# Kernel optimization log

Measured on AMD Instinct MI355X. Metric: run time of the kernel, lower is better.

## Reference

```python
import jax, jax.numpy as jnp
import numpy as np

LA, LB, D = 4096, 4096, 1024

def setup_inputs() -> dict:
    key = jax.random.key(0)
    ka, kb = jax.random.split(key)
    a_hat = jax.random.normal(ka, (LA, D), dtype=jnp.float32)
    b_hat = jax.random.normal(kb, (LB, D), dtype=jnp.float32)
    return {"a_hat": a_hat, "b_hat": b_hat}

def _m_vector(v_hat, v_wave):
    # concat along dim 0, matching torch.concat(..., dim=0)
    return jnp.concatenate((v_hat, v_wave, v_hat - v_wave, v_hat * v_wave), axis=0)

def reference(a_hat, b_hat):
    # energy: [La, Lb]
    energy = jnp.matmul(a_hat, b_hat.T)
    # softmax over columns (dim 1) -> attend over b rows
    wave_a = jnp.matmul(jax.nn.softmax(energy, axis=1), b_hat)      # [La, D]
    # softmax over rows (dim 0), transposed -> attend over a rows
    wave_b = jnp.matmul(jax.nn.softmax(energy, axis=0).T, a_hat)    # [Lb, D]
    m_a = _m_vector(a_hat, wave_a)   # [4*La, D]
    m_b = _m_vector(b_hat, wave_b)   # [4*Lb, D]
    return (m_a, m_b)
```

## Files before the change

kernel.cpp:

```cpp
#include <hip/hip_runtime.h>
#include <cstdint>
#include <cstddef>

#define LA 4096
#define LB 4096
#define DD 1024

typedef unsigned short u16;
typedef short bf16x8 __attribute__((ext_vector_type(8)));
typedef float f32x4 __attribute__((ext_vector_type(4)));

__device__ __forceinline__ u16 f2bf(float f) {
  unsigned u = __builtin_bit_cast(unsigned, f);
  u += 0x7fffu + ((u >> 16) & 1u);
  return (u16)(u >> 16);
}
__device__ __forceinline__ float bf2f(u16 h) {
  return __builtin_bit_cast(float, (unsigned)h << 16);
}
__device__ __forceinline__ void async16(const void* g, void* l) {
  __builtin_amdgcn_global_load_lds(
      (const __attribute__((address_space(1))) unsigned int*)g,
      (__attribute__((address_space(3))) unsigned int*)l, 16, 0, 0);
}

__global__ __launch_bounds__(256) void prep(const float* __restrict__ A,
                                            const float* __restrict__ B,
                                            u16* __restrict__ Ahi, u16* __restrict__ Alo,
                                            u16* __restrict__ Bhi, u16* __restrict__ Blo,
                                            u16* __restrict__ Bt) {
  __shared__ u16 t[32][33];
  const int bx = blockIdx.x;
  const int tid = threadIdx.x;
  if (bx < 4096) {
    const int side = bx >> 11;
    const size_t idx = ((size_t)(bx & 2047) * 256 + tid) * 8;
    const float* src = side ? B : A;
    u16* dh = side ? Bhi : Ahi;
    u16* dl = side ? Blo : Alo;
    const float4 a = *(const float4*)&src[idx];
    const float4 b = *(const float4*)&src[idx + 4];
    float v[8] = {a.x, a.y, a.z, a.w, b.x, b.y, b.z, b.w};
    bf16x8 hi, lo;
#pragma unroll
    for (int i = 0; i < 8; ++i) {
      const u16 h = f2bf(v[i]);
      hi[i] = (short)h;
      lo[i] = (short)f2bf(v[i] - bf2f(h));
    }
    *(bf16x8*)&dh[idx] = hi;
    *(bf16x8*)&dl[idx] = lo;
  } else {
    const int blk = bx - 4096;
    const int c0 = (blk & 31) * 32;
    const int r0 = (blk >> 5) * 32;
    const int lr = tid >> 3, lc = (tid & 7) * 4;
    const float4 v = *(const float4*)&B[(size_t)(r0 + lr) * DD + c0 + lc];
    t[lr][lc + 0] = f2bf(v.x); t[lr][lc + 1] = f2bf(v.y);
    t[lr][lc + 2] = f2bf(v.z); t[lr][lc + 3] = f2bf(v.w);
    __syncthreads();
    ushort4 w;
    w.x = t[lc + 0][lr]; w.y = t[lc + 1][lr]; w.z = t[lc + 2][lr]; w.w = t[lc + 3][lr];
    *(ushort4*)&Bt[(size_t)(c0 + lr) * LB + r0 + lc] = w;
  }
}

__global__ __launch_bounds__(256) void tr_f32(const float* __restrict__ in,
                                              u16* __restrict__ out,
                                              int R, int C) {
  __shared__ u16 t[32][33];
  const int c0 = blockIdx.x * 32, r0 = blockIdx.y * 32;
  const int tid = threadIdx.x;
  const int lr = tid >> 3, lc = (tid & 7) * 4;
  const float4 v = *(const float4*)&in[(size_t)(r0 + lr) * C + c0 + lc];
  t[lr][lc + 0] = f2bf(v.x); t[lr][lc + 1] = f2bf(v.y);
  t[lr][lc + 2] = f2bf(v.z); t[lr][lc + 3] = f2bf(v.w);
  __syncthreads();
  ushort4 w;
  w.x = t[lc + 0][lr]; w.y = t[lc + 1][lr]; w.z = t[lc + 2][lr]; w.w = t[lc + 3][lr];
  *(ushort4*)&out[(size_t)(c0 + lr) * R + r0 + lc] = w;
}

__global__ __launch_bounds__(256) void gemm_energy(const u16* __restrict__ Ahi,
                                                   const u16* __restrict__ Alo,
                                                   const u16* __restrict__ Bhi,
                                                   const u16* __restrict__ Blo,
                                                   float* __restrict__ E,
                                                   float* __restrict__ pmax,
                                                   float* __restrict__ psum) {
  __shared__ u16 lah[128 * 32], lal[128 * 32], lbh[128 * 32], lbl[128 * 32];
  __shared__ float cred[4][4][16][2];
  const int j0 = blockIdx.x * 128;
  const int i0 = blockIdx.y * 128;
  const int tid = threadIdx.x;
  const int lane = tid & 63, quad = lane >> 4, lq = lane & 15;
  const int wave = tid >> 6;
  const int wm = (wave & 1) * 64, wn = (wave >> 1) * 64;
  f32x4 acc[4][4] = {};
  for (int kt = 0; kt < DD; kt += 32) {
    if (kt) __syncthreads();
#pragma unroll
    for (int r = 0; r < 2; ++r) {
      const int chunk = wave * 128 + r * 64 + lane;
      const int row = chunk >> 2;
      const int kc = (chunk & 3) * 8;
      const int lofs = (wave * 128 + r * 64) * 16;
      const size_t ga = (size_t)(i0 + row) * DD + kt + kc;
      const size_t gb = (size_t)(j0 + row) * DD + kt + kc;
      async16(Ahi + ga, (char*)lah + lofs);
      async16(Alo + ga, (char*)lal + lofs);
      async16(Bhi + gb, (char*)lbh + lofs);
      async16(Blo + gb, (char*)lbl + lofs);
    }
    __syncthreads();
    bf16x8 fah[4], fal[4], fbh[4], fbl[4];
#pragma unroll
    for (int f = 0; f < 4; ++f) {
      fah[f] = *(const bf16x8*)&lah[(wm + f * 16 + lq) * 32 + quad * 8];
      fal[f] = *(const bf16x8*)&lal[(wm + f * 16 + lq) * 32 + quad * 8];
      fbh[f] = *(const bf16x8*)&lbh[(wn + f * 16 + lq) * 32 + quad * 8];
      fbl[f] = *(const bf16x8*)&lbl[(wn + f * 16 + lq) * 32 + quad * 8];
    }
#pragma unroll
    for (int fm = 0; fm < 4; ++fm)
#pragma unroll
      for (int fn = 0; fn < 4; ++fn) {
        acc[fm][fn] = __builtin_amdgcn_mfma_f32_16x16x32_bf16(fal[fm], fbh[fn], acc[fm][fn], 0, 0, 0);
        acc[fm][fn] = __builtin_amdgcn_mfma_f32_16x16x32_bf16(fah[fm], fbl[fn], acc[fm][fn], 0, 0, 0);
        acc[fm][fn] = __builtin_amdgcn_mfma_f32_16x16x32_bf16(fah[fm], fbh[fn], acc[fm][fn], 0, 0, 0);
      }
  }
#pragma unroll
  for (int fm = 0; fm < 4; ++fm)
#pragma unroll
    for (int fn = 0; fn < 4; ++fn)
#pragma unroll
      for (int r = 0; r < 4; ++r) {
        const int gi = i0 + wm + fm * 16 + quad * 4 + r;
        const int gj = j0 + wn + fn * 16 + lq;
        E[(size_t)gi * LB + gj] = acc[fm][fn][r];
      }
  const int rg = i0 >> 7;
#pragma unroll
  for (int fn = 0; fn < 4; ++fn) {
    float m = acc[0][fn][0];
#pragma unroll
    for (int fm = 0; fm < 4; ++fm)
#pragma unroll
      for (int r = 0; r < 4; ++r) m = fmaxf(m, acc[fm][fn][r]);
    float s = 0.f;
#pragma unroll
    for (int fm = 0; fm < 4; ++fm)
#pragma unroll
      for (int r = 0; r < 4; ++r) s += __expf(acc[fm][fn][r] - m);
#pragma unroll
    for (int mask = 16; mask <= 32; mask <<= 1) {
      const float om = __shfl_xor(m, mask);
      const float os = __shfl_xor(s, mask);
      const float nm = fmaxf(m, om);
      s = s * __expf(m - nm) + os * __expf(om - nm);
      m = nm;
    }
    if (quad == 0) { cred[wave][fn][lq][0] = m; cred[wave][fn][lq][1] = s; }
  }
  __syncthreads();
  if ((wave & 1) == 0 && quad == 0) {
#pragma unroll
    for (int fn = 0; fn < 4; ++fn) {
      const float m1 = cred[wave][fn][lq][0], s1 = cred[wave][fn][lq][1];
      const float m2 = cred[wave + 1][fn][lq][0], s2 = cred[wave + 1][fn][lq][1];
      const float nm = fmaxf(m1, m2);
      const float s = s1 * __expf(m1 - nm) + s2 * __expf(m2 - nm);
      const int c = j0 + wn + fn * 16 + lq;
      pmax[rg * LB + c] = nm;
      psum[rg * LB + c] = s;
    }
  }
}

__global__ __launch_bounds__(256) void row_softmax_pa(const float* __restrict__ E,
                                                      float* __restrict__ rinv,
                                                      u16* __restrict__ P,
                                                      float* __restrict__ wa) {
  __shared__ float red[8];
  const int row = blockIdx.x, tid = threadIdx.x;
  const float* e = E + (size_t)row * LB;
  float4 v[4];
#pragma unroll
  for (int c = 0; c < 4; ++c) v[c] = *(const float4*)&e[(c * 256 + tid) * 4];
  float m = -__builtin_inff();
#pragma unroll
  for (int c = 0; c < 4; ++c)
    m = fmaxf(m, fmaxf(fmaxf(v[c].x, v[c].y), fmaxf(v[c].z, v[c].w)));
#pragma unroll
  for (int o = 32; o > 0; o >>= 1) m = fmaxf(m, __shfl_down(m, o));
  if ((tid & 63) == 0) red[tid >> 6] = m;
  __syncthreads();
  m = fmaxf(fmaxf(red[0], red[1]), fmaxf(red[2], red[3]));
  float s = 0.f;
#pragma unroll
  for (int c = 0; c < 4; ++c)
    s += __expf(v[c].x - m) + __expf(v[c].y - m) + __expf(v[c].z - m) + __expf(v[c].w - m);
#pragma unroll
  for (int o = 32; o > 0; o >>= 1) s += __shfl_down(s, o);
  if ((tid & 63) == 0) red[4 + (tid >> 6)] = s;
  __syncthreads();
  if (tid == 0) rinv[row] = 1.f / (red[4] + red[5] + red[6] + red[7]);
#pragma unroll
  for (int c = 0; c < 4; ++c) {
    ushort4 w;
    w.x = f2bf(__expf(v[c].x - m));
    w.y = f2bf(__expf(v[c].y - m));
    w.z = f2bf(__expf(v[c].z - m));
    w.w = f2bf(__expf(v[c].w - m));
    *(ushort4*)&P[(size_t)row * LB + (c * 256 + tid) * 4] = w;
  }
  float4 z = {0.f, 0.f, 0.f, 0.f};
  *(float4*)&wa[(size_t)row * DD + tid * 4] = z;
}

__global__ __launch_bounds__(256) void col_combine(const float* __restrict__ pmax,
                                                   const float* __restrict__ psum,
                                                   float* __restrict__ cmax,
                                                   float* __restrict__ cinv) {
  const int c = blockIdx.x * 256 + threadIdx.x;
  float m = -__builtin_inff(), s = 0.f;
#pragma unroll 4
  for (int g = 0; g < 32; ++g) {
    const float pm = pmax[g * LB + c], ps = psum[g * LB + c];
    const float nm = fmaxf(m, pm);
    s = s * __expf(m - nm) + ps * __expf(pm - nm);
    m = nm;
  }
  cmax[c] = m;
  cinv[c] = 1.f / s;
}

__global__ __launch_bounds__(256) void make_pb(const float* __restrict__ E,
                                               const float* __restrict__ cmax,
                                               u16* __restrict__ P) {
  __shared__ u16 t[32][33];
  const int j0 = blockIdx.x * 32;
  const int i0 = blockIdx.y * 32;
  const int tid = threadIdx.x;
  const int lr = tid >> 3, lc = (tid & 7) * 4;
  const float4 v = *(const float4*)&E[(size_t)(i0 + lr) * LB + j0 + lc];
  const float4 cm = *(const float4*)&cmax[j0 + lc];
  t[lr][lc + 0] = f2bf(__expf(v.x - cm.x));
  t[lr][lc + 1] = f2bf(__expf(v.y - cm.y));
  t[lr][lc + 2] = f2bf(__expf(v.z - cm.z));
  t[lr][lc + 3] = f2bf(__expf(v.w - cm.w));
  __syncthreads();
  ushort4 w;
  w.x = t[lc + 0][lr]; w.y = t[lc + 1][lr]; w.z = t[lc + 2][lr]; w.w = t[lc + 3][lr];
  *(ushort4*)&P[(size_t)(j0 + lr) * LA + i0 + lc] = w;
}

template <int ATOMIC>
__global__ __launch_bounds__(256) void gemm_pv(const u16* __restrict__ P,
                                               const u16* __restrict__ Vt,
                                               const float* __restrict__ inv,
                                               float* __restrict__ W0,
                                               float* __restrict__ W1) {
  __shared__ u16 lds_a[128 * 32];
  __shared__ u16 lds_b[128 * 32];
  const int n0 = blockIdx.x * 128;
  const int i0 = blockIdx.y * 128;
  const int kz = blockIdx.z;
  const int tid = threadIdx.x;
  const int lane = tid & 63, quad = lane >> 4, lq = lane & 15;
  const int wave = tid >> 6;
  const int wm = (wave & 1) * 64, wn = (wave >> 1) * 64;
  f32x4 acc[4][4] = {};
  for (int t = 0; t < 64; ++t) {
    const int kt = kz * 2048 + t * 32;
    if (t) __syncthreads();
#pragma unroll
    for (int r = 0; r < 2; ++r) {
      const int chunk = wave * 128 + r * 64 + lane;
      const int row = chunk >> 2;
      const int kc = (chunk & 3) * 8;
      const int lofs = (wave * 128 + r * 64) * 16;
      async16(P + (size_t)(i0 + row) * 4096 + kt + kc, (char*)lds_a + lofs);
      async16(Vt + (size_t)(n0 + row) * 4096 + kt + kc, (char*)lds_b + lofs);
    }
    __syncthreads();
    bf16x8 af[4], bfr[4];
#pragma unroll
    for (int f = 0; f < 4; ++f) {
      af[f]  = *(const bf16x8*)&lds_a[(wm + f * 16 + lq) * 32 + quad * 8];
      bfr[f] = *(const bf16x8*)&lds_b[(wn + f * 16 + lq) * 32 + quad * 8];
    }
#pragma unroll
    for (int fm = 0; fm < 4; ++fm)
#pragma unroll
      for (int fn = 0; fn < 4; ++fn)
        acc[fm][fn] = __builtin_amdgcn_mfma_f32_16x16x32_bf16(af[fm], bfr[fn], acc[fm][fn], 0, 0, 0);
  }
  float* W = ATOMIC ? W0 : (kz ? W1 : W0);
#pragma unroll
  for (int fm = 0; fm < 4; ++fm)
#pragma unroll
    for (int r = 0; r < 4; ++r) {
      const int gm = i0 + wm + fm * 16 + quad * 4 + r;
      const float sc = inv[gm];
#pragma unroll
      for (int fn = 0; fn < 4; ++fn) {
        const int gn = n0 + wn + fn * 16 + lq;
        if (ATOMIC)
          unsafeAtomicAdd(&W[(size_t)gm * DD + gn], acc[fm][fn][r] * sc);
        else
          W[(size_t)gm * DD + gn] = acc[fm][fn][r] * sc;
      }
    }
}

__global__ __launch_bounds__(256) void finish(const float* __restrict__ Ain,
                                              const float* __restrict__ Bin,
                                              const float* __restrict__ p1,
                                              float* __restrict__ out) {
  const int side = blockIdx.x >> 11;
  const int blk = blockIdx.x & 2047;
  const size_t idx = ((size_t)blk * 256 + threadIdx.x) * 8;
  const size_t S = (size_t)LA * DD;
  const float* src = side ? Bin : Ain;
  float* ob = out + (size_t)side * 4 * S;
  const float4 a0 = *(const float4*)&src[idx];
  const float4 a1 = *(const float4*)&src[idx + 4];
  float4 w0 = *(const float4*)&ob[S + idx];
  float4 w1 = *(const float4*)&ob[S + idx + 4];
  if (side) {
    const float4 q0 = *(const float4*)&p1[idx];
    const float4 q1 = *(const float4*)&p1[idx + 4];
    w0.x += q0.x; w0.y += q0.y; w0.z += q0.z; w0.w += q0.w;
    w1.x += q1.x; w1.y += q1.y; w1.z += q1.z; w1.w += q1.w;
    *(float4*)&ob[S + idx] = w0;
    *(float4*)&ob[S + idx + 4] = w1;
  }
  float4 s0, s1, m0, m1;
  s0.x = a0.x - w0.x; s0.y = a0.y - w0.y; s0.z = a0.z - w0.z; s0.w = a0.w - w0.w;
  s1.x = a1.x - w1.x; s1.y = a1.y - w1.y; s1.z = a1.z - w1.z; s1.w = a1.w - w1.w;
  m0.x = a0.x * w0.x; m0.y = a0.y * w0.y; m0.z = a0.z * w0.z; m0.w = a0.w * w0.w;
  m1.x = a1.x * w1.x; m1.y = a1.y * w1.y; m1.z = a1.z * w1.z; m1.w = a1.w * w1.w;
  *(float4*)&ob[idx] = a0;            *(float4*)&ob[idx + 4] = a1;
  *(float4*)&ob[2 * S + idx] = s0;    *(float4*)&ob[2 * S + idx + 4] = s1;
  *(float4*)&ob[3 * S + idx] = m0;    *(float4*)&ob[3 * S + idx + 4] = m1;
}

extern "C" void kernel_launch(void* const* d_in, const int* in_sizes, int n_in,
                              void* d_out, int out_size, void* d_ws, size_t ws_size,
                              hipStream_t stream) {
  const float* A = (const float*)d_in[0];
  const float* B = (const float*)d_in[1];
  float* out = (float*)d_out;
  const size_t S = (size_t)LA * DD;

  float* pmax = out;
  float* psum = pmax + 131072;
  float* rmax = psum + 131072;
  float* rinv = rmax + 4096;
  float* cmax = rinv + 4096;
  float* cinv = cmax + 4096;
  u16*   Bt   = (u16*)(out + 1048576);
  u16*   Ahi  = (u16*)(out + 2 * S);
  u16*   Alo  = Ahi + S;
  u16*   Bhi  = Alo + S;
  u16*   Blo  = Bhi + S;
  u16*   P    = (u16*)(out + 2 * S);
  float* E    = out + 4 * S;
  u16*   At   = (u16*)(out + 4 * S);
  float* wave_a = out + S;
  float* wave_b = out + 5 * S;
  float* pB1    = out + 6 * S;

  prep<<<dim3(8192), 256, 0, stream>>>(A, B, Ahi, Alo, Bhi, Blo, Bt);

  gemm_energy<<<dim3(LB / 128, LA / 128), 256, 0, stream>>>(Ahi, Alo, Bhi, Blo, E, pmax, psum);

  row_softmax_pa<<<dim3(LA), 256, 0, stream>>>(E, rinv, P, wave_a);
  col_combine<<<dim3(LB / 256), 256, 0, stream>>>(pmax, psum, cmax, cinv);

  gemm_pv<1><<<dim3(DD / 128, LA / 128, 2), 256, 0, stream>>>(P, Bt, rinv, wave_a, nullptr);

  make_pb<<<dim3(LB / 32, LA / 32), 256, 0, stream>>>(E, cmax, P);
  tr_f32<<<dim3(DD / 32, LA / 32), 256, 0, stream>>>(A, At, LA, DD);
  gemm_pv<0><<<dim3(DD / 128, LB / 128, 2), 256, 0, stream>>>(P, At, cinv, wave_b, pB1);

  finish<<<dim3(4096), 256, 0, stream>>>(A, B, pB1, out);
}
```

Before: 442.2 us.

## Restructure energy GEMM with concatenated split-bf16 operands and 256x256 pipelined tiles

The split-bf16 hi/lo planes are interleaved into a single K=3072 operand per matrix: A becomes [hi,hi,lo] and B becomes [hi,lo,hi], so the three-product fp32 emulation turns into one plain bf16 GEMM. The energy kernel is rewritten as a 512-thread, 256x256-tile kernel with double-buffered LDS, an XOR swizzle against bank conflicts, interleaved load/MFMA phases with explicit barriers and priority hints, and a block-index swizzle for L2 locality. This targets global/LDS traffic and MFMA under-utilisation in the old 128x128 kernel. The cost is larger prep writes and more complex manual synchronisation, which could hide ordering bugs.

```diff
diff --git a/kernel.cpp b/kernel.cpp
--- a/kernel.cpp
+++ b/kernel.cpp
@@ -26,8 +26,8 @@
 
 __global__ __launch_bounds__(256) void prep(const float* __restrict__ A,
                                             const float* __restrict__ B,
-                                            u16* __restrict__ Ahi, u16* __restrict__ Alo,
-                                            u16* __restrict__ Bhi, u16* __restrict__ Blo,
+                                            u16* __restrict__ Ap,
+                                            u16* __restrict__ Bp,
                                             u16* __restrict__ Bt) {
   __shared__ u16 t[32][33];
   const int bx = blockIdx.x;
@@ -36,8 +36,7 @@
     const int side = bx >> 11;
     const size_t idx = ((size_t)(bx & 2047) * 256 + tid) * 8;
     const float* src = side ? B : A;
-    u16* dh = side ? Bhi : Ahi;
-    u16* dl = side ? Blo : Alo;
+    u16* dst = side ? Bp : Ap;
     const float4 a = *(const float4*)&src[idx];
     const float4 b = *(const float4*)&src[idx + 4];
     float v[8] = {a.x, a.y, a.z, a.w, b.x, b.y, b.z, b.w};
@@ -48,8 +47,12 @@
       hi[i] = (short)h;
       lo[i] = (short)f2bf(v[i] - bf2f(h));
     }
-    *(bf16x8*)&dh[idx] = hi;
-    *(bf16x8*)&dl[idx] = lo;
+    const size_t row = idx >> 10;
+    const size_t k = idx & 1023;
+    u16* base = dst + row * 3072 + k;
+    *(bf16x8*)&base[0] = hi;
+    *(bf16x8*)&base[side ? 2048 : 1024] = hi;
+    *(bf16x8*)&base[side ? 1024 : 2048] = lo;
   } else {
     const int blk = bx - 4096;
     const int c0 = (blk & 31) * 32;
@@ -81,76 +84,140 @@
   *(ushort4*)&out[(size_t)(c0 + lr) * R + r0 + lc] = w;
 }
 
-__global__ __launch_bounds__(256) void gemm_energy(const u16* __restrict__ Ahi,
-                                                   const u16* __restrict__ Alo,
-                                                   const u16* __restrict__ Bhi,
-                                                   const u16* __restrict__ Blo,
-                                                   float* __restrict__ E,
-                                                   float* __restrict__ pmax,
-                                                   float* __restrict__ psum) {
-  __shared__ u16 lah[128 * 32], lal[128 * 32], lbh[128 * 32], lbl[128 * 32];
-  __shared__ float cred[4][4][16][2];
-  const int j0 = blockIdx.x * 128;
-  const int i0 = blockIdx.y * 128;
+#define NTILES 48
+
+#define STAGE(M, h, tt)                                                      \
+  do {                                                                       \
+    if ((tt) < NTILES) {                                                     \
+      u16* lb = &lds[(tt) & 1][M][h][0];                                     \
+      async16(gsrc[M][h][0] + (tt) * 128, lb + ldst0);                       \
+      async16(gsrc[M][h][1] + (tt) * 128, lb + ldst1);                       \
+    }                                                                        \
+  } while (0)
+
+#define LDA(mbase)                                                           \
+  _Pragma("unroll") for (int m = 0; m < 4; ++m)                              \
+  _Pragma("unroll") for (int ks = 0; ks < 2; ++ks) {                         \
+    const int row = (mbase + m) * 16 + lq;                                   \
+    const int cb = (ks * 64 + quad * 16) ^ (((row >> 2) & 1) << 5);          \
+    af[m][ks] = *(const bf16x8*)&lds[p][0][wr][row * 64 + (cb >> 1)];        \
+  }
+
+#define LDB(arr, fbase)                                                      \
+  _Pragma("unroll") for (int f = 0; f < 2; ++f)                              \
+  _Pragma("unroll") for (int ks = 0; ks < 2; ++ks) {                         \
+    const int row = (wc & 1) * 64 + (fbase + f) * 16 + lq;                   \
+    const int cb = (ks * 64 + quad * 16) ^ (((row >> 2) & 1) << 5);          \
+    arr[f][ks] = *(const bf16x8*)&lds[p][1][wc >> 1][row * 64 + (cb >> 1)];  \
+  }
+
+#define MM(mbase, fbase, barr)                                               \
+  __builtin_amdgcn_s_setprio(1);                                             \
+  _Pragma("unroll") for (int m = 0; m < 4; ++m)                              \
+  _Pragma("unroll") for (int f = 0; f < 2; ++f)                              \
+  _Pragma("unroll") for (int ks = 0; ks < 2; ++ks)                           \
+    acc[mbase + m][fbase + f] = __builtin_amdgcn_mfma_f32_16x16x32_bf16(     \
+        af[m][ks], barr[f][ks], acc[mbase + m][fbase + f], 0, 0, 0);         \
+  __builtin_amdgcn_s_setprio(0);
+
+#define SBAR __builtin_amdgcn_s_barrier()
+#define SCHB __builtin_amdgcn_sched_barrier(0)
+#define LGKM0 asm volatile("s_waitcnt lgkmcnt(0)" ::: "memory")
+
+__global__ __launch_bounds__(512, 2) void gemm8ph(const u16* __restrict__ Ap,
+                                                  const u16* __restrict__ Bp,
+                                                  float* __restrict__ E,
+                                                  float* __restrict__ pmax,
+                                                  float* __restrict__ psum) {
+  __shared__ u16 lds[2][2][2][8192];
   const int tid = threadIdx.x;
   const int lane = tid & 63, quad = lane >> 4, lq = lane & 15;
   const int wave = tid >> 6;
-  const int wm = (wave & 1) * 64, wn = (wave >> 1) * 64;
-  f32x4 acc[4][4] = {};
-  for (int kt = 0; kt < DD; kt += 32) {
-    if (kt) __syncthreads();
-#pragma unroll
-    for (int r = 0; r < 2; ++r) {
-      const int chunk = wave * 128 + r * 64 + lane;
-      const int row = chunk >> 2;
-      const int kc = (chunk & 3) * 8;
-      const int lofs = (wave * 128 + r * 64) * 16;
-      const size_t ga = (size_t)(i0 + row) * DD + kt + kc;
-      const size_t gb = (size_t)(j0 + row) * DD + kt + kc;
-      async16(Ahi + ga, (char*)lah + lofs);
-      async16(Alo + ga, (char*)lal + lofs);
-      async16(Bhi + gb, (char*)lbh + lofs);
-      async16(Blo + gb, (char*)lbl + lofs);
-    }
-    __syncthreads();
-    bf16x8 fah[4], fal[4], fbh[4], fbl[4];
-#pragma unroll
-    for (int f = 0; f < 4; ++f) {
-      fah[f] = *(const bf16x8*)&lah[(wm + f * 16 + lq) * 32 + quad * 8];
-      fal[f] = *(const bf16x8*)&lal[(wm + f * 16 + lq) * 32 + quad * 8];
-      fbh[f] = *(const bf16x8*)&lbh[(wn + f * 16 + lq) * 32 + quad * 8];
-      fbl[f] = *(const bf16x8*)&lbl[(wn + f * 16 + lq) * 32 + quad * 8];
-    }
-#pragma unroll
-    for (int fm = 0; fm < 4; ++fm)
-#pragma unroll
-      for (int fn = 0; fn < 4; ++fn) {
-        acc[fm][fn] = __builtin_amdgcn_mfma_f32_16x16x32_bf16(fal[fm], fbh[fn], acc[fm][fn], 0, 0, 0);
-        acc[fm][fn] = __builtin_amdgcn_mfma_f32_16x16x32_bf16(fah[fm], fbl[fn], acc[fm][fn], 0, 0, 0);
-        acc[fm][fn] = __builtin_amdgcn_mfma_f32_16x16x32_bf16(fah[fm], fbh[fn], acc[fm][fn], 0, 0, 0);
+  const int wr = wave >> 2, wc = wave & 3;
+  int lin = blockIdx.y * 16 + blockIdx.x;
+  lin = (lin & 7) * 32 + (lin >> 3);
+  const int j0 = (lin & 15) * 256;
+  const int i0 = (lin >> 4) * 256;
+
+  const char* gsrc[2][2][2];
+  int ldst0, ldst1;
+  {
+    const int db0 = tid * 16, db1 = 8192 + tid * 16;
+    const int dr0 = db0 >> 7, dr1 = db1 >> 7;
+    const int sc0 = (db0 & 127) ^ (((dr0 >> 2) & 1) << 5);
+    const int sc1 = (db1 & 127) ^ (((dr1 >> 2) & 1) << 5);
+    ldst0 = wave * 512;
+    ldst1 = 4096 + wave * 512;
+#pragma unroll
+    for (int M = 0; M < 2; ++M)
+#pragma unroll
+      for (int h = 0; h < 2; ++h) {
+        const char* base = (const char*)(M ? Bp : Ap);
+        const int rb = (M ? j0 : i0) + h * 128;
+        gsrc[M][h][0] = base + (size_t)(rb + dr0) * 6144 + sc0;
+        gsrc[M][h][1] = base + (size_t)(rb + dr1) * 6144 + sc1;
       }
   }
-#pragma unroll
-  for (int fm = 0; fm < 4; ++fm)
+
+  f32x4 acc[8][4] = {};
+  bf16x8 af[4][2], bf0[2][2], bf1[2][2];
+
+  STAGE(1, 0, 0); STAGE(1, 1, 0); STAGE(0, 0, 0); STAGE(0, 1, 0);
+  asm volatile("s_waitcnt vmcnt(4)" ::: "memory");
+  STAGE(1, 0, 1); STAGE(1, 1, 1); STAGE(0, 0, 1);
+  asm volatile("s_waitcnt vmcnt(6)" ::: "memory");
+  SBAR;
+
+  for (int t = 0; t < NTILES; ++t) {
+    const int p = t & 1;
+    SCHB;
+    LDA(0); LDB(bf0, 0);
+    STAGE(0, 1, t + 1);
+    SCHB; SBAR; LGKM0; SCHB;
+    MM(0, 0, bf0);
+    SCHB; SBAR;
+    SCHB;
+    LDB(bf1, 2);
+    STAGE(1, 0, t + 2);
+    SCHB; SBAR; LGKM0; SCHB;
+    MM(0, 2, bf1);
+    SCHB; SBAR;
+    SCHB;
+    LDA(4);
+    STAGE(1, 1, t + 2);
+    SCHB; SBAR; LGKM0; SCHB;
+    MM(4, 0, bf0);
+    SCHB; SBAR;
+    SCHB;
+    STAGE(0, 0, t + 2);
+    SCHB; SBAR; LGKM0; SCHB;
+    MM(4, 2, bf1);
+    SCHB;
+    asm volatile("s_waitcnt vmcnt(6)" ::: "memory");
+    SBAR;
+  }
+
+  const int rbase = i0 + wr * 128;
+  const int cbase = j0 + wc * 64;
+#pragma unroll
+  for (int fm = 0; fm < 8; ++fm)
 #pragma unroll
     for (int fn = 0; fn < 4; ++fn)
 #pragma unroll
-      for (int r = 0; r < 4; ++r) {
-        const int gi = i0 + wm + fm * 16 + quad * 4 + r;
-        const int gj = j0 + wn + fn * 16 + lq;
-        E[(size_t)gi * LB + gj] = acc[fm][fn][r];
-      }
-  const int rg = i0 >> 7;
+      for (int r = 0; r < 4; ++r)
+        E[(size_t)(rbase + fm * 16 + quad * 4 + r) * LB + cbase + fn * 16 + lq] =
+            acc[fm][fn][r];
+  const int rg = (i0 >> 7) + wr;
 #pragma unroll
   for (int fn = 0; fn < 4; ++fn) {
     float m = acc[0][fn][0];
 #pragma unroll
-    for (int fm = 0; fm < 4; ++fm)
+    for (int fm = 0; fm < 8; ++fm)
 #pragma unroll
       for (int r = 0; r < 4; ++r) m = fmaxf(m, acc[fm][fn][r]);
     float s = 0.f;
 #pragma unroll
-    for (int fm = 0; fm < 4; ++fm)
+    for (int fm = 0; fm < 8; ++fm)
 #pragma unroll
       for (int r = 0; r < 4; ++r) s += __expf(acc[fm][fn][r] - m);
 #pragma unroll
@@ -161,19 +228,9 @@
       s = s * __expf(m - nm) + os * __expf(om - nm);
       m = nm;
     }
-    if (quad == 0) { cred[wave][fn][lq][0] = m; cred[wave][fn][lq][1] = s; }
-  }
-  __syncthreads();
-  if ((wave & 1) == 0 && quad == 0) {
-#pragma unroll
-    for (int fn = 0; fn < 4; ++fn) {
-      const float m1 = cred[wave][fn][lq][0], s1 = cred[wave][fn][lq][1];
-      const float m2 = cred[wave + 1][fn][lq][0], s2 = cred[wave + 1][fn][lq][1];
-      const float nm = fmaxf(m1, m2);
-      const float s = s1 * __expf(m1 - nm) + s2 * __expf(m2 - nm);
-      const int c = j0 + wn + fn * 16 + lq;
-      pmax[rg * LB + c] = nm;
-      psum[rg * LB + c] = s;
+    if (quad == 0) {
+      pmax[rg * LB + cbase + fn * 16 + lq] = m;
+      psum[rg * LB + cbase + fn * 16 + lq] = s;
     }
   }
 }
@@ -362,10 +419,8 @@
   float* cmax = rinv + 4096;
   float* cinv = cmax + 4096;
   u16*   Bt   = (u16*)(out + 1048576);
-  u16*   Ahi  = (u16*)(out + 2 * S);
-  u16*   Alo  = Ahi + S;
-  u16*   Bhi  = Alo + S;
-  u16*   Blo  = Bhi + S;
+  u16*   Ap   = (u16*)(out + S);
+  u16*   Bp   = Ap + (size_t)LA * 3072;
   u16*   P    = (u16*)(out + 2 * S);
   float* E    = out + 4 * S;
   u16*   At   = (u16*)(out + 4 * S);
@@ -373,9 +428,9 @@
   float* wave_b = out + 5 * S;
   float* pB1    = out + 6 * S;
 
-  prep<<<dim3(8192), 256, 0, stream>>>(A, B, Ahi, Alo, Bhi, Blo, Bt);
-
-  gemm_energy<<<dim3(LB / 128, LA / 128), 256, 0, stream>>>(Ahi, Alo, Bhi, Blo, E, pmax, psum);
+  prep<<<dim3(8192), 256, 0, stream>>>(A, B, Ap, Bp, Bt);
+
+  gemm8ph<<<dim3(16, 16), 512, 0, stream>>>(Ap, Bp, E, pmax, psum);
 
   row_softmax_pa<<<dim3(LA), 256, 0, stream>>>(E, rinv, P, wave_a);
   col_combine<<<dim3(LB / 256), 256, 0, stream>>>(pmax, psum, cmax, cinv);
```

New measurement: 440.0 us. About the same (-0.5%).
